# Performance work log

Hardware: AMD Instinct MI355X
Metric: run time of the kernel (lower is better)

## Reference

```python
import jax, jax.numpy as jnp
import numpy as np

N = 50000        # nodes
E = 800000       # edges (before self-loops)
IN_DIM = 128
HID = 32         # per-head hidden channels, conv1
OUT = 32         # per-head output channels, conv2
H = 4            # attention heads
NEG_SLOPE = 0.2  # PyG GATConv default


def setup_inputs() -> dict:
    key = jax.random.key(0)
    ks = jax.random.split(key, 12)
    x = jax.random.normal(ks[0], (N, IN_DIM), dtype=jnp.float32)
    edge_index = jax.random.randint(ks[1], (2, E), 0, N, dtype=jnp.int32)
    s = 0.05
    W1 = jax.random.normal(ks[2], (IN_DIM, H * HID), dtype=jnp.float32) * s
    a_src1 = jax.random.normal(ks[3], (H, HID), dtype=jnp.float32) * s
    a_dst1 = jax.random.normal(ks[4], (H, HID), dtype=jnp.float32) * s
    b1 = jnp.zeros((H * HID,), dtype=jnp.float32)
    W2 = jax.random.normal(ks[5], (H * HID, H * OUT), dtype=jnp.float32) * s
    a_src2 = jax.random.normal(ks[6], (H, OUT), dtype=jnp.float32) * s
    a_dst2 = jax.random.normal(ks[7], (H, OUT), dtype=jnp.float32) * s
    b2 = jnp.zeros((H * OUT,), dtype=jnp.float32)
    return {"x": x, "edge_index": edge_index,
            "W1": W1, "a_src1": a_src1, "a_dst1": a_dst1, "b1": b1,
            "W2": W2, "a_src2": a_src2, "a_dst2": a_dst2, "b2": b2}


def _gat_conv(x, src, dst, W, a_src, a_dst, b, heads, ch):
    # linear transform: [N, heads, ch]
    h = (x @ W).reshape(-1, heads, ch)
    # per-node attention logits [N, heads]
    al_src = jnp.einsum('nhc,hc->nh', h, a_src)
    al_dst = jnp.einsum('nhc,hc->nh', h, a_dst)
    # per-edge logits, leaky relu  [Etot, heads]
    e = jax.nn.leaky_relu(al_src[src] + al_dst[dst], negative_slope=NEG_SLOPE)
    # softmax over incoming edges of each destination node
    m = jax.lax.stop_gradient(jax.ops.segment_max(e, dst, num_segments=N))
    ex = jnp.exp(e - m[dst])
    denom = jax.ops.segment_sum(ex, dst, num_segments=N)
    alpha = ex / denom[dst]                      # [Etot, heads]
    # weighted scatter-aggregate of source features
    out = jax.ops.segment_sum(alpha[:, :, None] * h[src], dst, num_segments=N)
    return out.reshape(N, heads * ch) + b


def reference(x, edge_index, W1, a_src1, a_dst1, b1, W2, a_src2, a_dst2, b2):
    # PyG GATConv add_self_loops=True
    loops = jnp.arange(N, dtype=edge_index.dtype)
    src = jnp.concatenate([edge_index[0], loops])
    dst = jnp.concatenate([edge_index[1], loops])
    # eval mode: dropout is identity
    h = _gat_conv(x, src, dst, W1, a_src1, a_dst1, b1, H, HID)
    h = jax.nn.elu(h)
    out = _gat_conv(h, src, dst, W2, a_src2, a_dst2, b2, H, OUT)
    return out
```

## Files before the change

### kernel.cpp

```cpp
#include <hip/hip_runtime.h>
#include <hip/hip_bf16.h>

#define NN 50000
#define EE 800000
#define ETOT (EE + NN)
#define F 128
#define HEADS 4
#define MT 64
#define NB ((NN + 1023) / 1024)

typedef __bf16 bf16x8 __attribute__((ext_vector_type(8)));
typedef float  f32x4  __attribute__((ext_vector_type(4)));

__device__ __forceinline__ unsigned short f32_to_bf16(float f) {
    unsigned int u = __float_as_uint(f);
    u += 0x7fffu + ((u >> 16) & 1u);
    return (unsigned short)(u >> 16);
}
__device__ __forceinline__ float bf16bits_to_f32(unsigned short s) {
    return __uint_as_float(((unsigned int)s) << 16);
}
__device__ __forceinline__ float bflo(unsigned int u) { return __uint_as_float(u << 16); }
__device__ __forceinline__ float bfhi(unsigned int u) { return __uint_as_float(u & 0xffff0000u); }

union BU { unsigned short u[8]; bf16x8 v; };


__global__ void wpack_k(const float* __restrict__ W1, const float* __restrict__ W2,
                        unsigned short* __restrict__ wf) {
    int t = blockIdx.x * blockDim.x + threadIdx.x;
    if (t >= 2 * 2048) return;
    int which = t >> 11;
    int rem = t & 2047;
    int lane = rem & 63;
    int tile = rem >> 6;
    int kt = tile >> 3, nt = tile & 7;
    int q = lane >> 4, c = lane & 15;
    const float* W = which ? W2 : W1;
    BU vh, vl;
#pragma unroll
    for (int j = 0; j < 8; j++) {
        float w = W[(kt * 32 + q * 8 + j) * F + nt * 16 + c];
        unsigned short hb = f32_to_bf16(w);
        vh.u[j] = hb;
        vl.u[j] = f32_to_bf16(w - bf16bits_to_f32(hb));
    }
    size_t base_h = ((size_t)(which * 2 + 0) * 2048 + tile * 64 + lane) * 8;
    size_t base_l = ((size_t)(which * 2 + 1) * 2048 + tile * 64 + lane) * 8;
    *(bf16x8*)&wf[base_h] = vh.v;
    *(bf16x8*)&wf[base_l] = vl.v;
}


__launch_bounds__(256)
__global__ void gemm_mfma(const float* __restrict__ A, const unsigned short* __restrict__ wf,
                          const float* __restrict__ a_src, const float* __restrict__ a_dst,
                          unsigned short* __restrict__ Cb, float* __restrict__ als,
                          float* __restrict__ ald, int M,
                          const int* __restrict__ ei, int* __restrict__ counts,
                          int* __restrict__ pos, int gemm_blocks) {
    __shared__ unsigned char smem[65536];
    int tid = threadIdx.x;
    int w = tid >> 6, lane = tid & 63;
    int m = lane & 15, q = lane >> 4;
    int row0 = blockIdx.x * MT + w * 16;

    {
        const uint4* src = (const uint4*)wf;
        uint4* dst = (uint4*)smem;
#pragma unroll
        for (int i = 0; i < 16; i++) dst[tid + i * 256] = src[tid + i * 256];
    }
    __syncthreads();

    int ar = row0 + m; if (ar >= M) ar = 0;
    const float* arow = A + (size_t)ar * F + q * 8;
    const unsigned short* lds_h = (const unsigned short*)smem;
    const unsigned short* lds_l = (const unsigned short*)(smem + 32768);

    f32x4 acc[8];
#pragma unroll
    for (int nt = 0; nt < 8; nt++) acc[nt] = (f32x4){0.f, 0.f, 0.f, 0.f};

#pragma unroll
    for (int kt = 0; kt < 4; kt++) {
        float4 a0 = *(const float4*)(arow + kt * 32);
        float4 a1 = *(const float4*)(arow + kt * 32 + 4);
        float av[8] = {a0.x, a0.y, a0.z, a0.w, a1.x, a1.y, a1.z, a1.w};
        BU ah, al;
#pragma unroll
        for (int j = 0; j < 8; j++) {
            unsigned short hb = f32_to_bf16(av[j]);
            ah.u[j] = hb;
            al.u[j] = f32_to_bf16(av[j] - bf16bits_to_f32(hb));
        }
#pragma unroll
        for (int nt = 0; nt < 8; nt++) {
            int bo = ((kt * 8 + nt) * 64 + lane) * 8;
            bf16x8 bh = *(const bf16x8*)&lds_h[bo];
            bf16x8 bl = *(const bf16x8*)&lds_l[bo];
            acc[nt] = __builtin_amdgcn_mfma_f32_16x16x32_bf16(ah.v, bh, acc[nt], 0, 0, 0);
            acc[nt] = __builtin_amdgcn_mfma_f32_16x16x32_bf16(al.v, bh, acc[nt], 0, 0, 0);
            acc[nt] = __builtin_amdgcn_mfma_f32_16x16x32_bf16(ah.v, bl, acc[nt], 0, 0, 0);
        }
    }
    __syncthreads();

    float* L = (float*)smem + w * (16 * 132);
#pragma unroll
    for (int nt = 0; nt < 8; nt++)
#pragma unroll
        for (int r = 0; r < 4; r++)
            L[(q * 4 + r) * 132 + nt * 16 + m] = acc[nt][r];

    int rr = lane >> 2;
    int head = lane & 3;
    int c0 = head * 32;
    int gr = row0 + rr;
    float v[32];
#pragma unroll
    for (int i = 0; i < 8; i++)
        *(float4*)&v[i * 4] = *(const float4*)&L[rr * 132 + c0 + i * 4];

    if (gr < M) {
#pragma unroll
        for (int i = 0; i < 4; i++) {
            uint4 pk;
            pk.x = (unsigned)f32_to_bf16(v[i * 8 + 0]) | ((unsigned)f32_to_bf16(v[i * 8 + 1]) << 16);
            pk.y = (unsigned)f32_to_bf16(v[i * 8 + 2]) | ((unsigned)f32_to_bf16(v[i * 8 + 3]) << 16);
            pk.z = (unsigned)f32_to_bf16(v[i * 8 + 4]) | ((unsigned)f32_to_bf16(v[i * 8 + 5]) << 16);
            pk.w = (unsigned)f32_to_bf16(v[i * 8 + 6]) | ((unsigned)f32_to_bf16(v[i * 8 + 7]) << 16);
            *(uint4*)&Cb[(size_t)gr * F + c0 + i * 8] = pk;
        }
        float ps = 0.f, pd = 0.f;
#pragma unroll
        for (int i = 0; i < 32; i++) {
            ps += v[i] * a_src[c0 + i];
            pd += v[i] * a_dst[c0 + i];
        }
        als[gr * HEADS + head] = ps;
        ald[gr * HEADS + head] = pd;
    }

    if (ei) {
        int stride = gemm_blocks * 256;
        for (int e = blockIdx.x * 256 + tid; e < ETOT; e += stride) {
            int dst = (e < EE) ? ei[EE + e] : (e - EE);
            pos[e] = atomicAdd(&counts[dst], 1);
        }
    }
}


__launch_bounds__(1024)
__global__ void scan_block_k(const int* __restrict__ counts, int* __restrict__ row_ptr,
                             int* __restrict__ bsum, int n) {
    int tid = threadIdx.x;
    int i = blockIdx.x * 1024 + tid;
    int v = (i < n) ? counts[i] : 0;
    int lane = tid & 63;
    int wave = tid >> 6;
    int x = v;
#pragma unroll
    for (int off = 1; off < 64; off <<= 1) {
        int t = __shfl_up(x, off, 64);
        if (lane >= off) x += t;
    }
    __shared__ int wsum[16];
    if (lane == 63) wsum[wave] = x;
    __syncthreads();
    if (wave == 0) {
        int w = (lane < 16) ? wsum[lane] : 0;
#pragma unroll
        for (int off = 1; off < 16; off <<= 1) {
            int t = __shfl_up(w, off, 64);
            if (lane >= off) w += t;
        }
        if (lane < 16) wsum[lane] = w;
    }
    __syncthreads();
    int base = (wave > 0) ? wsum[wave - 1] : 0;
    int incl = base + x;
    if (i < n) row_ptr[i] = incl - v;
    if (tid == 1023) bsum[blockIdx.x] = incl;
}

__launch_bounds__(256)
__global__ void scan_add_k(int* __restrict__ row_ptr, const int* __restrict__ bsum, int n) {
    __shared__ int off_s[NB];
    if (threadIdx.x < 64) {
        int lane = threadIdx.x;
        int v = (lane < NB) ? bsum[lane] : 0;
        int x = v;
#pragma unroll
        for (int o = 1; o < 64; o <<= 1) {
            int t = __shfl_up(x, o, 64);
            if (lane >= o) x += t;
        }
        if (lane < NB) off_s[lane] = x - v;
    }
    __syncthreads();
    int i = blockIdx.x * blockDim.x + threadIdx.x;
    if (i < n) row_ptr[i] += off_s[i >> 10];
    if (i == 0) row_ptr[n] = ETOT;
}

__global__ void fill_k(const int* __restrict__ ei, const int* __restrict__ row_ptr,
                       const int* __restrict__ pos, int* __restrict__ csr_src) {
    int e = blockIdx.x * blockDim.x + threadIdx.x;
    if (e >= ETOT) return;
    int src, dst;
    if (e < EE) { src = ei[e]; dst = ei[EE + e]; }
    else        { src = e - EE; dst = e - EE; }
    csr_src[row_ptr[dst] + pos[e]] = src;
}


__launch_bounds__(256)
__global__ void aggregate(const unsigned short* __restrict__ hb, const float* __restrict__ als,
                          const float* __restrict__ ald, const int* __restrict__ row_ptr,
                          const int* __restrict__ csr_src, const float* __restrict__ bias,
                          float* __restrict__ out, int apply_elu) {
    int wave = threadIdx.x >> 6;
    int n = blockIdx.x * 4 + wave;
    if (n >= NN) return;
    int lane = threadIdx.x & 63;
    int g  = lane >> 4;
    int cl = lane & 15;
    int head = cl >> 2;
    float aldv = ald[n * HEADS + head];
    int jb = row_ptr[n], je = row_ptr[n + 1];

    float acc[8];
#pragma unroll
    for (int i = 0; i < 8; i++) acc[i] = 0.f;
    float den = 0.f;

    int j = jb + g;
    for (; j + 4 < je; j += 8) {
        int s0 = csr_src[j];
        int s1 = csr_src[j + 4];
        float e0 = als[s0 * HEADS + head] + aldv;
        float e1 = als[s1 * HEADS + head] + aldv;
        uint4 r0 = *(const uint4*)&hb[(size_t)s0 * F + cl * 8];
        uint4 r1 = *(const uint4*)&hb[(size_t)s1 * F + cl * 8];
        e0 = (e0 > 0.f) ? e0 : 0.2f * e0;
        e1 = (e1 > 0.f) ? e1 : 0.2f * e1;
        float p0 = __expf(e0);
        float p1 = __expf(e1);
        den += p0 + p1;
        acc[0] += p0 * bflo(r0.x); acc[1] += p0 * bfhi(r0.x);
        acc[2] += p0 * bflo(r0.y); acc[3] += p0 * bfhi(r0.y);
        acc[4] += p0 * bflo(r0.z); acc[5] += p0 * bfhi(r0.z);
        acc[6] += p0 * bflo(r0.w); acc[7] += p0 * bfhi(r0.w);
        acc[0] += p1 * bflo(r1.x); acc[1] += p1 * bfhi(r1.x);
        acc[2] += p1 * bflo(r1.y); acc[3] += p1 * bfhi(r1.y);
        acc[4] += p1 * bflo(r1.z); acc[5] += p1 * bfhi(r1.z);
        acc[6] += p1 * bflo(r1.w); acc[7] += p1 * bfhi(r1.w);
    }
    if (j < je) {
        int s = csr_src[j];
        float e = als[s * HEADS + head] + aldv;
        uint4 raw = *(const uint4*)&hb[(size_t)s * F + cl * 8];
        e = (e > 0.f) ? e : 0.2f * e;
        float p = __expf(e);
        den += p;
        acc[0] += p * bflo(raw.x); acc[1] += p * bfhi(raw.x);
        acc[2] += p * bflo(raw.y); acc[3] += p * bfhi(raw.y);
        acc[4] += p * bflo(raw.z); acc[5] += p * bfhi(raw.z);
        acc[6] += p * bflo(raw.w); acc[7] += p * bfhi(raw.w);
    }

#pragma unroll
    for (int i = 0; i < 8; i++) {
        acc[i] += __shfl_xor(acc[i], 16);
        acc[i] += __shfl_xor(acc[i], 32);
    }
    den += __shfl_xor(den, 16);
    den += __shfl_xor(den, 32);

    if (g == 0) {
        float inv = 1.f / den;
        float v[8];
#pragma unroll
        for (int i = 0; i < 8; i++) {
            v[i] = acc[i] * inv + bias[cl * 8 + i];
            if (apply_elu) v[i] = (v[i] > 0.f) ? v[i] : (__expf(v[i]) - 1.f);
        }
        float4* op = (float4*)&out[(size_t)n * F + cl * 8];
        op[0] = make_float4(v[0], v[1], v[2], v[3]);
        op[1] = make_float4(v[4], v[5], v[6], v[7]);
    }
}


extern "C" void kernel_launch(void* const* d_in, const int* in_sizes, int n_in,
                              void* d_out, int out_size, void* d_ws, size_t ws_size,
                              hipStream_t stream) {
    const float* x   = (const float*)d_in[0];
    const int*   ei  = (const int*)d_in[1];
    const float* W1  = (const float*)d_in[2];
    const float* as1 = (const float*)d_in[3];
    const float* ad1 = (const float*)d_in[4];
    const float* b1  = (const float*)d_in[5];
    const float* W2  = (const float*)d_in[6];
    const float* as2 = (const float*)d_in[7];
    const float* ad2 = (const float*)d_in[8];
    const float* b2  = (const float*)d_in[9];
    float* out = (float*)d_out;

    char* ws = (char*)d_ws;
    size_t off = 0;
    auto alloc = [&](size_t bytes) {
        void* p = ws + off;
        off += (bytes + 255) & ~(size_t)255;
        return p;
    };
    unsigned short* hb = (unsigned short*)alloc((size_t)NN * F * 2);
    float* als     = (float*)alloc((size_t)NN * HEADS * 4);
    float* ald     = (float*)alloc((size_t)NN * HEADS * 4);
    int*   counts  = (int*)alloc((size_t)NN * 4);
    int*   row_ptr = (int*)alloc((size_t)(NN + 1) * 4);
    int*   bsum    = (int*)alloc((size_t)NB * 4);
    int*   csr_src = (int*)alloc((size_t)ETOT * 4);
    int*   pos     = (int*)alloc((size_t)ETOT * 4);
    unsigned short* wf = (unsigned short*)alloc((size_t)4 * 2048 * 8 * 2);

    int GG = (NN + MT - 1) / MT;
    int agg_grid = (NN + 3) / 4;

    (void)hipMemsetAsync(counts, 0, (size_t)NN * 4, stream);
    wpack_k<<<16, 256, 0, stream>>>(W1, W2, wf);

    gemm_mfma<<<GG, 256, 0, stream>>>(x, wf, as1, ad1, hb, als, ald, NN,
                                      ei, counts, pos, GG);
    scan_block_k<<<NB, 1024, 0, stream>>>(counts, row_ptr, bsum, NN);
    scan_add_k<<<(NN + 255) / 256, 256, 0, stream>>>(row_ptr, bsum, NN);
    fill_k<<<(ETOT + 255) / 256, 256, 0, stream>>>(ei, row_ptr, pos, csr_src);
    aggregate<<<agg_grid, 256, 0, stream>>>(hb, als, ald, row_ptr, csr_src, b1, out, 1);

    gemm_mfma<<<GG, 256, 0, stream>>>(out, wf + (size_t)2 * 2048 * 8, as2, ad2, hb, als, ald, NN,
                                      (const int*)nullptr, (int*)nullptr, (int*)nullptr, GG);
    aggregate<<<agg_grid, 256, 0, stream>>>(hb, als, ald, row_ptr, csr_src, b2, out, 0);
}
```

Before: 267.3 us.

## Process four row tiles per wave in GEMM to amortize weight staging

Each block now handles 256 rows instead of 64: every wave computes four 16-row tiles, reusing each LDS weight fragment across four MFMA row tiles. A-row loads for the next k-step are software-prefetched into registers, and the first loads are issued before the barrier so they overlap the LDS fill. This cuts the number of blocks that copy the 64KB packed weights into LDS by a factor of four. The cost is much higher register pressure (128 accumulator floats per lane), a launch bound capping occupancy at one block, and fewer blocks for the edge-count atomics loop to spread across.

```diff
diff --git a/kernel.cpp b/kernel.cpp
--- a/kernel.cpp
+++ b/kernel.cpp
@@ -6,7 +6,7 @@
 #define ETOT (EE + NN)
 #define F 128
 #define HEADS 4
-#define MT 64
+#define RPB 256
 #define NB ((NN + 1023) / 1024)
 
 typedef __bf16 bf16x8 __attribute__((ext_vector_type(8)));
@@ -52,7 +52,7 @@
 }
 
 
-__launch_bounds__(256)
+__launch_bounds__(256, 1)
 __global__ void gemm_mfma(const float* __restrict__ A, const unsigned short* __restrict__ wf,
                           const float* __restrict__ a_src, const float* __restrict__ a_dst,
                           unsigned short* __restrict__ Cb, float* __restrict__ als,
@@ -63,7 +63,7 @@
     int tid = threadIdx.x;
     int w = tid >> 6, lane = tid & 63;
     int m = lane & 15, q = lane >> 4;
-    int row0 = blockIdx.x * MT + w * 16;
+    int row0 = blockIdx.x * RPB + w * 64;
 
     {
         const uint4* src = (const uint4*)wf;
@@ -71,75 +71,109 @@
 #pragma unroll
         for (int i = 0; i < 16; i++) dst[tid + i * 256] = src[tid + i * 256];
     }
-    __syncthreads();
-
-    int ar = row0 + m; if (ar >= M) ar = 0;
-    const float* arow = A + (size_t)ar * F + q * 8;
+
+    const float* ap[4];
+#pragma unroll
+    for (int rt = 0; rt < 4; rt++) {
+        int ar = row0 + rt * 16 + m;
+        if (ar >= M) ar = 0;
+        ap[rt] = A + (size_t)ar * F + q * 8;
+    }
+    float4 a0[4], a1[4];
+#pragma unroll
+    for (int rt = 0; rt < 4; rt++) {
+        a0[rt] = *(const float4*)(ap[rt]);
+        a1[rt] = *(const float4*)(ap[rt] + 4);
+    }
+    __syncthreads();
+
     const unsigned short* lds_h = (const unsigned short*)smem;
     const unsigned short* lds_l = (const unsigned short*)(smem + 32768);
 
-    f32x4 acc[8];
-#pragma unroll
-    for (int nt = 0; nt < 8; nt++) acc[nt] = (f32x4){0.f, 0.f, 0.f, 0.f};
+    f32x4 acc[8][4];
+#pragma unroll
+    for (int nt = 0; nt < 8; nt++)
+#pragma unroll
+        for (int rt = 0; rt < 4; rt++) acc[nt][rt] = (f32x4){0.f, 0.f, 0.f, 0.f};
 
 #pragma unroll
     for (int kt = 0; kt < 4; kt++) {
-        float4 a0 = *(const float4*)(arow + kt * 32);
-        float4 a1 = *(const float4*)(arow + kt * 32 + 4);
-        float av[8] = {a0.x, a0.y, a0.z, a0.w, a1.x, a1.y, a1.z, a1.w};
-        BU ah, al;
-#pragma unroll
-        for (int j = 0; j < 8; j++) {
-            unsigned short hb = f32_to_bf16(av[j]);
-            ah.u[j] = hb;
-            al.u[j] = f32_to_bf16(av[j] - bf16bits_to_f32(hb));
+        float4 n0[4], n1[4];
+        if (kt < 3) {
+#pragma unroll
+            for (int rt = 0; rt < 4; rt++) {
+                n0[rt] = *(const float4*)(ap[rt] + (kt + 1) * 32);
+                n1[rt] = *(const float4*)(ap[rt] + (kt + 1) * 32 + 4);
+            }
+        }
+        BU ah[4], al[4];
+#pragma unroll
+        for (int rt = 0; rt < 4; rt++) {
+            float av[8] = {a0[rt].x, a0[rt].y, a0[rt].z, a0[rt].w,
+                           a1[rt].x, a1[rt].y, a1[rt].z, a1[rt].w};
+#pragma unroll
+            for (int j = 0; j < 8; j++) {
+                unsigned short hb = f32_to_bf16(av[j]);
+                ah[rt].u[j] = hb;
+                al[rt].u[j] = f32_to_bf16(av[j] - bf16bits_to_f32(hb));
+            }
         }
 #pragma unroll
         for (int nt = 0; nt < 8; nt++) {
             int bo = ((kt * 8 + nt) * 64 + lane) * 8;
             bf16x8 bh = *(const bf16x8*)&lds_h[bo];
             bf16x8 bl = *(const bf16x8*)&lds_l[bo];
-            acc[nt] = __builtin_amdgcn_mfma_f32_16x16x32_bf16(ah.v, bh, acc[nt], 0, 0, 0);
-            acc[nt] = __builtin_amdgcn_mfma_f32_16x16x32_bf16(al.v, bh, acc[nt], 0, 0, 0);
-            acc[nt] = __builtin_amdgcn_mfma_f32_16x16x32_bf16(ah.v, bl, acc[nt], 0, 0, 0);
+#pragma unroll
+            for (int rt = 0; rt < 4; rt++) {
+                acc[nt][rt] = __builtin_amdgcn_mfma_f32_16x16x32_bf16(ah[rt].v, bh, acc[nt][rt], 0, 0, 0);
+                acc[nt][rt] = __builtin_amdgcn_mfma_f32_16x16x32_bf16(al[rt].v, bh, acc[nt][rt], 0, 0, 0);
+                acc[nt][rt] = __builtin_amdgcn_mfma_f32_16x16x32_bf16(ah[rt].v, bl, acc[nt][rt], 0, 0, 0);
+            }
+        }
+        if (kt < 3) {
+#pragma unroll
+            for (int rt = 0; rt < 4; rt++) { a0[rt] = n0[rt]; a1[rt] = n1[rt]; }
         }
     }
     __syncthreads();
 
     float* L = (float*)smem + w * (16 * 132);
-#pragma unroll
-    for (int nt = 0; nt < 8; nt++)
-#pragma unroll
-        for (int r = 0; r < 4; r++)
-            L[(q * 4 + r) * 132 + nt * 16 + m] = acc[nt][r];
-
     int rr = lane >> 2;
     int head = lane & 3;
     int c0 = head * 32;
-    int gr = row0 + rr;
-    float v[32];
-#pragma unroll
-    for (int i = 0; i < 8; i++)
-        *(float4*)&v[i * 4] = *(const float4*)&L[rr * 132 + c0 + i * 4];
-
-    if (gr < M) {
-#pragma unroll
-        for (int i = 0; i < 4; i++) {
-            uint4 pk;
-            pk.x = (unsigned)f32_to_bf16(v[i * 8 + 0]) | ((unsigned)f32_to_bf16(v[i * 8 + 1]) << 16);
-            pk.y = (unsigned)f32_to_bf16(v[i * 8 + 2]) | ((unsigned)f32_to_bf16(v[i * 8 + 3]) << 16);
-            pk.z = (unsigned)f32_to_bf16(v[i * 8 + 4]) | ((unsigned)f32_to_bf16(v[i * 8 + 5]) << 16);
-            pk.w = (unsigned)f32_to_bf16(v[i * 8 + 6]) | ((unsigned)f32_to_bf16(v[i * 8 + 7]) << 16);
-            *(uint4*)&Cb[(size_t)gr * F + c0 + i * 8] = pk;
-        }
-        float ps = 0.f, pd = 0.f;
-#pragma unroll
-        for (int i = 0; i < 32; i++) {
-            ps += v[i] * a_src[c0 + i];
-            pd += v[i] * a_dst[c0 + i];
-        }
-        als[gr * HEADS + head] = ps;
-        ald[gr * HEADS + head] = pd;
+#pragma unroll
+    for (int rt = 0; rt < 4; rt++) {
+#pragma unroll
+        for (int nt = 0; nt < 8; nt++)
+#pragma unroll
+            for (int r = 0; r < 4; r++)
+                L[(q * 4 + r) * 132 + nt * 16 + m] = acc[nt][rt][r];
+
+        int gr = row0 + rt * 16 + rr;
+        float v[32];
+#pragma unroll
+        for (int i = 0; i < 8; i++)
+            *(float4*)&v[i * 4] = *(const float4*)&L[rr * 132 + c0 + i * 4];
+
+        if (gr < M) {
+#pragma unroll
+            for (int i = 0; i < 4; i++) {
+                uint4 pk;
+                pk.x = (unsigned)f32_to_bf16(v[i * 8 + 0]) | ((unsigned)f32_to_bf16(v[i * 8 + 1]) << 16);
+                pk.y = (unsigned)f32_to_bf16(v[i * 8 + 2]) | ((unsigned)f32_to_bf16(v[i * 8 + 3]) << 16);
+                pk.z = (unsigned)f32_to_bf16(v[i * 8 + 4]) | ((unsigned)f32_to_bf16(v[i * 8 + 5]) << 16);
+                pk.w = (unsigned)f32_to_bf16(v[i * 8 + 6]) | ((unsigned)f32_to_bf16(v[i * 8 + 7]) << 16);
+                *(uint4*)&Cb[(size_t)gr * F + c0 + i * 8] = pk;
+            }
+            float ps = 0.f, pd = 0.f;
+#pragma unroll
+            for (int i = 0; i < 32; i++) {
+                ps += v[i] * a_src[c0 + i];
+                pd += v[i] * a_dst[c0 + i];
+            }
+            als[gr * HEADS + head] = ps;
+            ald[gr * HEADS + head] = pd;
+        }
     }
 
     if (ei) {
@@ -326,7 +360,7 @@
     int*   pos     = (int*)alloc((size_t)ETOT * 4);
     unsigned short* wf = (unsigned short*)alloc((size_t)4 * 2048 * 8 * 2);
 
-    int GG = (NN + MT - 1) / MT;
+    int GG = (NN + RPB - 1) / RPB;
     int agg_grid = (NN + 3) / 4;
 
     (void)hipMemsetAsync(counts, 0, (size_t)NN * 4, stream);
```

New measurement: 276.2 us. 1.03x slower.

## Map one node per 16-lane group in aggregate and enlarge GEMM blocks to 512 threads

Applied to the files above, without the earlier changes.

The aggregation kernel now assigns each 16-lane group its own destination node and walks its edges serially with 4-way unrolling. This replaces one node per wave with edge groups combined by cross-lane shuffles, removing the reductions and idle lanes in the epilogue. The risk is longer per-node serial chains and divergence between groups with different degrees. The GEMM kernel uses 512-thread blocks covering 128 rows, halving the repeated weight staging into LDS. It prefetches the A rows before the barrier and runs the epilogue in two phases because of LDS capacity.

```diff
diff --git a/kernel.cpp b/kernel.cpp
--- a/kernel.cpp
+++ b/kernel.cpp
@@ -6,7 +6,7 @@
 #define ETOT (EE + NN)
 #define F 128
 #define HEADS 4
-#define MT 64
+#define RPB 128
 #define NB ((NN + 1023) / 1024)
 
 typedef __bf16 bf16x8 __attribute__((ext_vector_type(8)));
@@ -52,7 +52,7 @@
 }
 
 
-__launch_bounds__(256)
+__launch_bounds__(512, 4)
 __global__ void gemm_mfma(const float* __restrict__ A, const unsigned short* __restrict__ wf,
                           const float* __restrict__ a_src, const float* __restrict__ a_dst,
                           unsigned short* __restrict__ Cb, float* __restrict__ als,
@@ -63,18 +63,25 @@
     int tid = threadIdx.x;
     int w = tid >> 6, lane = tid & 63;
     int m = lane & 15, q = lane >> 4;
-    int row0 = blockIdx.x * MT + w * 16;
+    int row0 = blockIdx.x * RPB + w * 16;
 
     {
         const uint4* src = (const uint4*)wf;
         uint4* dst = (uint4*)smem;
 #pragma unroll
-        for (int i = 0; i < 16; i++) dst[tid + i * 256] = src[tid + i * 256];
-    }
-    __syncthreads();
+        for (int i = 0; i < 8; i++) dst[tid + i * 512] = src[tid + i * 512];
+    }
 
     int ar = row0 + m; if (ar >= M) ar = 0;
     const float* arow = A + (size_t)ar * F + q * 8;
+    float4 a0[4], a1[4];
+#pragma unroll
+    for (int kt = 0; kt < 4; kt++) {
+        a0[kt] = *(const float4*)(arow + kt * 32);
+        a1[kt] = *(const float4*)(arow + kt * 32 + 4);
+    }
+    __syncthreads();
+
     const unsigned short* lds_h = (const unsigned short*)smem;
     const unsigned short* lds_l = (const unsigned short*)(smem + 32768);
 
@@ -84,9 +91,8 @@
 
 #pragma unroll
     for (int kt = 0; kt < 4; kt++) {
-        float4 a0 = *(const float4*)(arow + kt * 32);
-        float4 a1 = *(const float4*)(arow + kt * 32 + 4);
-        float av[8] = {a0.x, a0.y, a0.z, a0.w, a1.x, a1.y, a1.z, a1.w};
+        float av[8] = {a0[kt].x, a0[kt].y, a0[kt].z, a0[kt].w,
+                       a1[kt].x, a1[kt].y, a1[kt].z, a1[kt].w};
         BU ah, al;
 #pragma unroll
         for (int j = 0; j < 8; j++) {
@@ -106,45 +112,48 @@
     }
     __syncthreads();
 
-    float* L = (float*)smem + w * (16 * 132);
-#pragma unroll
-    for (int nt = 0; nt < 8; nt++)
-#pragma unroll
-        for (int r = 0; r < 4; r++)
-            L[(q * 4 + r) * 132 + nt * 16 + m] = acc[nt][r];
-
     int rr = lane >> 2;
     int head = lane & 3;
     int c0 = head * 32;
     int gr = row0 + rr;
-    float v[32];
-#pragma unroll
-    for (int i = 0; i < 8; i++)
-        *(float4*)&v[i * 4] = *(const float4*)&L[rr * 132 + c0 + i * 4];
-
-    if (gr < M) {
-#pragma unroll
-        for (int i = 0; i < 4; i++) {
-            uint4 pk;
-            pk.x = (unsigned)f32_to_bf16(v[i * 8 + 0]) | ((unsigned)f32_to_bf16(v[i * 8 + 1]) << 16);
-            pk.y = (unsigned)f32_to_bf16(v[i * 8 + 2]) | ((unsigned)f32_to_bf16(v[i * 8 + 3]) << 16);
-            pk.z = (unsigned)f32_to_bf16(v[i * 8 + 4]) | ((unsigned)f32_to_bf16(v[i * 8 + 5]) << 16);
-            pk.w = (unsigned)f32_to_bf16(v[i * 8 + 6]) | ((unsigned)f32_to_bf16(v[i * 8 + 7]) << 16);
-            *(uint4*)&Cb[(size_t)gr * F + c0 + i * 8] = pk;
-        }
-        float ps = 0.f, pd = 0.f;
-#pragma unroll
-        for (int i = 0; i < 32; i++) {
-            ps += v[i] * a_src[c0 + i];
-            pd += v[i] * a_dst[c0 + i];
-        }
-        als[gr * HEADS + head] = ps;
-        ald[gr * HEADS + head] = pd;
+    for (int phase = 0; phase < 2; phase++) {
+        if ((w >> 2) == phase) {
+            float* L = (float*)smem + (w & 3) * (16 * 132);
+#pragma unroll
+            for (int nt = 0; nt < 8; nt++)
+#pragma unroll
+                for (int r = 0; r < 4; r++)
+                    L[(q * 4 + r) * 132 + nt * 16 + m] = acc[nt][r];
+            float v[32];
+#pragma unroll
+            for (int i = 0; i < 8; i++)
+                *(float4*)&v[i * 4] = *(const float4*)&L[rr * 132 + c0 + i * 4];
+            if (gr < M) {
+#pragma unroll
+                for (int i = 0; i < 4; i++) {
+                    uint4 pk;
+                    pk.x = (unsigned)f32_to_bf16(v[i * 8 + 0]) | ((unsigned)f32_to_bf16(v[i * 8 + 1]) << 16);
+                    pk.y = (unsigned)f32_to_bf16(v[i * 8 + 2]) | ((unsigned)f32_to_bf16(v[i * 8 + 3]) << 16);
+                    pk.z = (unsigned)f32_to_bf16(v[i * 8 + 4]) | ((unsigned)f32_to_bf16(v[i * 8 + 5]) << 16);
+                    pk.w = (unsigned)f32_to_bf16(v[i * 8 + 6]) | ((unsigned)f32_to_bf16(v[i * 8 + 7]) << 16);
+                    *(uint4*)&Cb[(size_t)gr * F + c0 + i * 8] = pk;
+                }
+                float ps = 0.f, pd = 0.f;
+#pragma unroll
+                for (int i = 0; i < 32; i++) {
+                    ps += v[i] * a_src[c0 + i];
+                    pd += v[i] * a_dst[c0 + i];
+                }
+                als[gr * HEADS + head] = ps;
+                ald[gr * HEADS + head] = pd;
+            }
+        }
+        __syncthreads();
     }
 
     if (ei) {
-        int stride = gemm_blocks * 256;
-        for (int e = blockIdx.x * 256 + tid; e < ETOT; e += stride) {
+        int stride = gemm_blocks * 512;
+        for (int e = blockIdx.x * 512 + tid; e < ETOT; e += stride) {
             int dst = (e < EE) ? ei[EE + e] : (e - EE);
             pos[e] = atomicAdd(&counts[dst], 1);
         }
@@ -221,12 +230,11 @@
                           const float* __restrict__ ald, const int* __restrict__ row_ptr,
                           const int* __restrict__ csr_src, const float* __restrict__ bias,
                           float* __restrict__ out, int apply_elu) {
-    int wave = threadIdx.x >> 6;
-    int n = blockIdx.x * 4 + wave;
-    if (n >= NN) return;
-    int lane = threadIdx.x & 63;
+    int tid = threadIdx.x;
+    int lane = tid & 63;
     int g  = lane >> 4;
     int cl = lane & 15;
+    int n = blockIdx.x * 16 + (tid >> 6) * 4 + g;
     int head = cl >> 2;
     float aldv = ald[n * HEADS + head];
     int jb = row_ptr[n], je = row_ptr[n + 1];
@@ -236,19 +244,27 @@
     for (int i = 0; i < 8; i++) acc[i] = 0.f;
     float den = 0.f;
 
-    int j = jb + g;
-    for (; j + 4 < je; j += 8) {
+    int j = jb;
+    for (; j + 3 < je; j += 4) {
         int s0 = csr_src[j];
-        int s1 = csr_src[j + 4];
-        float e0 = als[s0 * HEADS + head] + aldv;
-        float e1 = als[s1 * HEADS + head] + aldv;
+        int s1 = csr_src[j + 1];
+        int s2 = csr_src[j + 2];
+        int s3 = csr_src[j + 3];
+        float e0 = als[s0 * HEADS + head];
+        float e1 = als[s1 * HEADS + head];
+        float e2 = als[s2 * HEADS + head];
+        float e3 = als[s3 * HEADS + head];
         uint4 r0 = *(const uint4*)&hb[(size_t)s0 * F + cl * 8];
         uint4 r1 = *(const uint4*)&hb[(size_t)s1 * F + cl * 8];
+        uint4 r2 = *(const uint4*)&hb[(size_t)s2 * F + cl * 8];
+        uint4 r3 = *(const uint4*)&hb[(size_t)s3 * F + cl * 8];
+        e0 += aldv; e1 += aldv; e2 += aldv; e3 += aldv;
         e0 = (e0 > 0.f) ? e0 : 0.2f * e0;
         e1 = (e1 > 0.f) ? e1 : 0.2f * e1;
-        float p0 = __expf(e0);
-        float p1 = __expf(e1);
-        den += p0 + p1;
+        e2 = (e2 > 0.f) ? e2 : 0.2f * e2;
+        e3 = (e3 > 0.f) ? e3 : 0.2f * e3;
+        float p0 = __expf(e0), p1 = __expf(e1), p2 = __expf(e2), p3 = __expf(e3);
+        den += (p0 + p1) + (p2 + p3);
         acc[0] += p0 * bflo(r0.x); acc[1] += p0 * bfhi(r0.x);
         acc[2] += p0 * bflo(r0.y); acc[3] += p0 * bfhi(r0.y);
         acc[4] += p0 * bflo(r0.z); acc[5] += p0 * bfhi(r0.z);
@@ -257,8 +273,16 @@
         acc[2] += p1 * bflo(r1.y); acc[3] += p1 * bfhi(r1.y);
         acc[4] += p1 * bflo(r1.z); acc[5] += p1 * bfhi(r1.z);
         acc[6] += p1 * bflo(r1.w); acc[7] += p1 * bfhi(r1.w);
-    }
-    if (j < je) {
+        acc[0] += p2 * bflo(r2.x); acc[1] += p2 * bfhi(r2.x);
+        acc[2] += p2 * bflo(r2.y); acc[3] += p2 * bfhi(r2.y);
+        acc[4] += p2 * bflo(r2.z); acc[5] += p2 * bfhi(r2.z);
+        acc[6] += p2 * bflo(r2.w); acc[7] += p2 * bfhi(r2.w);
+        acc[0] += p3 * bflo(r3.x); acc[1] += p3 * bfhi(r3.x);
+        acc[2] += p3 * bflo(r3.y); acc[3] += p3 * bfhi(r3.y);
+        acc[4] += p3 * bflo(r3.z); acc[5] += p3 * bfhi(r3.z);
+        acc[6] += p3 * bflo(r3.w); acc[7] += p3 * bfhi(r3.w);
+    }
+    for (; j < je; j++) {
         int s = csr_src[j];
         float e = als[s * HEADS + head] + aldv;
         uint4 raw = *(const uint4*)&hb[(size_t)s * F + cl * 8];
@@ -271,26 +295,16 @@
         acc[6] += p * bflo(raw.w); acc[7] += p * bfhi(raw.w);
     }
 
+    float inv = 1.f / den;
+    float v[8];
 #pragma unroll
     for (int i = 0; i < 8; i++) {
-        acc[i] += __shfl_xor(acc[i], 16);
-        acc[i] += __shfl_xor(acc[i], 32);
-    }
-    den += __shfl_xor(den, 16);
-    den += __shfl_xor(den, 32);
-
-    if (g == 0) {
-        float inv = 1.f / den;
-        float v[8];
-#pragma unroll
-        for (int i = 0; i < 8; i++) {
-            v[i] = acc[i] * inv + bias[cl * 8 + i];
-            if (apply_elu) v[i] = (v[i] > 0.f) ? v[i] : (__expf(v[i]) - 1.f);
-        }
-        float4* op = (float4*)&out[(size_t)n * F + cl * 8];
-        op[0] = make_float4(v[0], v[1], v[2], v[3]);
-        op[1] = make_float4(v[4], v[5], v[6], v[7]);
-    }
+        v[i] = acc[i] * inv + bias[cl * 8 + i];
+        if (apply_elu) v[i] = (v[i] > 0.f) ? v[i] : (__expf(v[i]) - 1.f);
+    }
+    float4* op = (float4*)&out[(size_t)n * F + cl * 8];
+    op[0] = make_float4(v[0], v[1], v[2], v[3]);
+    op[1] = make_float4(v[4], v[5], v[6], v[7]);
 }
 
 
@@ -326,20 +340,20 @@
     int*   pos     = (int*)alloc((size_t)ETOT * 4);
     unsigned short* wf = (unsigned short*)alloc((size_t)4 * 2048 * 8 * 2);
 
-    int GG = (NN + MT - 1) / MT;
-    int agg_grid = (NN + 3) / 4;
+    int GG = (NN + RPB - 1) / RPB;
+    int agg_grid = (NN + 15) / 16;
 
     (void)hipMemsetAsync(counts, 0, (size_t)NN * 4, stream);
     wpack_k<<<16, 256, 0, stream>>>(W1, W2, wf);
 
-    gemm_mfma<<<GG, 256, 0, stream>>>(x, wf, as1, ad1, hb, als, ald, NN,
+    gemm_mfma<<<GG, 512, 0, stream>>>(x, wf, as1, ad1, hb, als, ald, NN,
                                       ei, counts, pos, GG);
     scan_block_k<<<NB, 1024, 0, stream>>>(counts, row_ptr, bsum, NN);
     scan_add_k<<<(NN + 255) / 256, 256, 0, stream>>>(row_ptr, bsum, NN);
     fill_k<<<(ETOT + 255) / 256, 256, 0, stream>>>(ei, row_ptr, pos, csr_src);
     aggregate<<<agg_grid, 256, 0, stream>>>(hb, als, ald, row_ptr, csr_src, b1, out, 1);
 
-    gemm_mfma<<<GG, 256, 0, stream>>>(out, wf + (size_t)2 * 2048 * 8, as2, ad2, hb, als, ald, NN,
+    gemm_mfma<<<GG, 512, 0, stream>>>(out, wf + (size_t)2 * 2048 * 8, as2, ad2, hb, als, ald, NN,
                                       (const int*)nullptr, (int*)nullptr, (int*)nullptr, GG);
     aggregate<<<agg_grid, 256, 0, stream>>>(hb, als, ald, row_ptr, csr_src, b2, out, 0);
 }
```

New measurement: 261.7 us. -2.1%, faster.
